# Optimization experiments

Measured on AMD Instinct MI355X. Metric: run time of the kernel, lower is better.

The kernel has to match this reference:

```python
import jax, jax.numpy as jnp
import numpy as np

B, S, HID = 1, 4096, 2048
HQ, HKV, D = 16, 8, 128
G = HQ // HKV
WINDOW = 1024
EPS = 1e-6
ROPE_THETA = 1e6


def setup_inputs() -> dict:
    key = jax.random.key(0)
    ks = jax.random.split(key, 6)
    hidden_states = jax.random.normal(ks[0], (B, S, HID), dtype=jnp.float32)
    Wq = jax.random.normal(ks[1], (HQ * D, HID), dtype=jnp.float32) * 0.02
    Wk = jax.random.normal(ks[2], (HKV * D, HID), dtype=jnp.float32) * 0.02
    Wv = jax.random.normal(ks[3], (HKV * D, HID), dtype=jnp.float32) * 0.02
    Wo = jax.random.normal(ks[4], (HID, HQ * D), dtype=jnp.float32) * 0.02
    q_norm_w = jnp.ones((D,), dtype=jnp.float32)
    k_norm_w = jnp.ones((D,), dtype=jnp.float32)
    # standard RoPE tables
    inv_freq = 1.0 / (ROPE_THETA ** (jnp.arange(0, D, 2, dtype=jnp.float32) / D))
    pos = jnp.arange(S, dtype=jnp.float32)
    freqs = pos[:, None] * inv_freq[None, :]            # [S, D/2]
    emb = jnp.concatenate([freqs, freqs], axis=-1)       # [S, D]
    cos = jnp.cos(emb)[None]                             # [1, S, D]
    sin = jnp.sin(emb)[None]
    return {"hidden_states": hidden_states, "cos": cos, "sin": sin,
            "Wq": Wq, "Wk": Wk, "Wv": Wv, "Wo": Wo,
            "q_norm_w": q_norm_w, "k_norm_w": k_norm_w}


def _rms_norm(x, w):
    var = jnp.mean(jnp.square(x), axis=-1, keepdims=True)
    return w * (x * jax.lax.rsqrt(var + EPS))


def _rotate_half(x):
    x1, x2 = jnp.split(x, 2, axis=-1)
    return jnp.concatenate([-x2, x1], axis=-1)


def reference(hidden_states, cos, sin, Wq, Wk, Wv, Wo, q_norm_w, k_norm_w):
    b, s, _ = hidden_states.shape
    # projections -> [B, H, S, D]
    q = (hidden_states @ Wq.T).reshape(b, s, HQ, D)
    k = (hidden_states @ Wk.T).reshape(b, s, HKV, D)
    v = (hidden_states @ Wv.T).reshape(b, s, HKV, D)
    q = _rms_norm(q, q_norm_w).transpose(0, 2, 1, 3)   # [B,HQ,S,D]
    k = _rms_norm(k, k_norm_w).transpose(0, 2, 1, 3)   # [B,HKV,S,D]
    v = v.transpose(0, 2, 1, 3)
    # RoPE (cos/sin broadcast over head dim)
    c = cos[:, None, :, :]
    sn = sin[:, None, :, :]
    q = q * c + _rotate_half(q) * sn
    k = k * c + _rotate_half(k) * sn
    # GQA: group queries per kv head
    qg = q.reshape(b, HKV, G, s, D)
    scaling = D ** -0.5
    scores = jnp.einsum('bhgqd,bhkd->bhgqk', qg, k) * scaling  # [B,HKV,G,S,S]
    # causal + sliding-window additive mask
    i = jnp.arange(s)[:, None]
    j = jnp.arange(s)[None, :]
    allowed = (j <= i) & (j > i - WINDOW)
    scores = jnp.where(allowed[None, None, None], scores, jnp.float32(-1e9))
    attn = jax.nn.softmax(scores, axis=-1)
    out = jnp.einsum('bhgqk,bhkd->bhgqd', attn, v)     # [B,HKV,G,S,D]
    out = out.reshape(b, HQ, s, D).transpose(0, 2, 1, 3).reshape(b, s, HQ * D)
    return out @ Wo.T
```

## Files before the change

### kernel.cpp

```cpp
#include <hip/hip_runtime.h>

typedef __bf16 bf16;
typedef bf16 bf16x8 __attribute__((ext_vector_type(8)));
typedef bf16 bf16x4 __attribute__((ext_vector_type(4)));
typedef float f32x4 __attribute__((ext_vector_type(4)));

#define MFMA16(a, b, c) __builtin_amdgcn_mfma_f32_16x16x32_bf16((a), (b), (c), 0, 0, 0)

__device__ __forceinline__ void gload_lds16(const bf16* g, bf16* l) {
  __builtin_amdgcn_global_load_lds(
      (const __attribute__((address_space(1))) void*)g,
      (__attribute__((address_space(3))) void*)l, 16, 0, 0);
}

__global__ __launch_bounds__(256) void cvt_f32_bf16(const float* __restrict__ src,
                                                    bf16* __restrict__ dst, int n4) {
  int i = blockIdx.x * blockDim.x + threadIdx.x;
  if (i < n4) {
    float4 v = ((const float4*)src)[i];
    bf16x4 o;
    o[0] = (bf16)v.x; o[1] = (bf16)v.y; o[2] = (bf16)v.z; o[3] = (bf16)v.w;
    ((bf16x4*)dst)[i] = o;
  }
}

template <typename OutT>
__global__ __launch_bounds__(256) void gemm_bt(const bf16* __restrict__ A,
                                               const bf16* __restrict__ B,
                                               OutT* __restrict__ C,
                                               int M, int N, int K) {
  __shared__ __align__(16) bf16 As[128 * 64];
  __shared__ __align__(16) bf16 Bs[128 * 64];
  const int tid = threadIdx.x;
  const int w = tid >> 6, lane = tid & 63;
  const int l15 = lane & 15, quad = lane >> 4;
  const int m0 = blockIdx.y * 128, n0 = blockIdx.x * 128;
  const int wm = (w >> 1) * 64, wn = (w & 1) * 64;

  f32x4 acc[4][4] = {};

  for (int k0 = 0; k0 < K; k0 += 64) {
#pragma unroll
    for (int i = 0; i < 4; i++) {
      int s = w * 256 + i * 64 + lane;
      int row = s >> 3;
      int c8 = (s & 7) ^ (row & 7);
      gload_lds16(A + (size_t)(m0 + row) * K + k0 + c8 * 8, As + (w * 256 + i * 64) * 8);
    }
#pragma unroll
    for (int i = 0; i < 4; i++) {
      int s = w * 256 + i * 64 + lane;
      int row = s >> 3;
      int c8 = (s & 7) ^ (row & 7);
      gload_lds16(B + (size_t)(n0 + row) * K + k0 + c8 * 8, Bs + (w * 256 + i * 64) * 8);
    }
    __syncthreads();

#pragma unroll
    for (int kk = 0; kk < 2; kk++) {
      bf16x8 af[4], bfr[4];
#pragma unroll
      for (int mt = 0; mt < 4; mt++) {
        int row = wm + mt * 16 + l15;
        int slot = row * 8 + ((kk * 4 + quad) ^ (row & 7));
        af[mt] = *(const bf16x8*)(As + slot * 8);
      }
#pragma unroll
      for (int nt = 0; nt < 4; nt++) {
        int row = wn + nt * 16 + l15;
        int slot = row * 8 + ((kk * 4 + quad) ^ (row & 7));
        bfr[nt] = *(const bf16x8*)(Bs + slot * 8);
      }
#pragma unroll
      for (int mt = 0; mt < 4; mt++)
#pragma unroll
        for (int nt = 0; nt < 4; nt++)
          acc[mt][nt] = MFMA16(af[mt], bfr[nt], acc[mt][nt]);
    }
    __syncthreads();
  }

#pragma unroll
  for (int mt = 0; mt < 4; mt++)
#pragma unroll
    for (int nt = 0; nt < 4; nt++) {
      int row = m0 + wm + mt * 16 + quad * 4;
      int col = n0 + wn + nt * 16 + l15;
#pragma unroll
      for (int r = 0; r < 4; r++)
        C[(size_t)(row + r) * N + col] = (OutT)acc[mt][nt][r];
    }
}

__global__ __launch_bounds__(256) void normrope(const bf16* __restrict__ QKVb,
                                                const float* __restrict__ cosb,
                                                const float* __restrict__ sinb,
                                                const float* __restrict__ qw,
                                                const float* __restrict__ kw,
                                                bf16* __restrict__ Qb,
                                                bf16* __restrict__ Kb) {
  const int wid = (blockIdx.x * blockDim.x + threadIdx.x) >> 6;
  const int lane = threadIdx.x & 63;
  const int s = wid / 24;
  const int h = wid % 24;
  const bool isq = (h < 16);
  const int col0 = isq ? h * 128 : 2048 + (h - 16) * 128;
  const float* wt = isq ? qw : kw;

  const bf16* row = QKVb + (size_t)s * 4096 + col0;
  float x1 = (float)row[lane];
  float x2 = (float)row[lane + 64];

  float ss = x1 * x1 + x2 * x2;
#pragma unroll
  for (int m = 32; m >= 1; m >>= 1) ss += __shfl_xor(ss, m, 64);
  float rs = rsqrtf(ss * (1.0f / 128.0f) + 1e-6f);

  float c = cosb[(size_t)s * 128 + lane];
  float sn = sinb[(size_t)s * 128 + lane];
  float xn1 = x1 * rs * wt[lane];
  float xn2 = x2 * rs * wt[lane + 64];
  float o1 = xn1 * c - xn2 * sn;
  float o2 = xn2 * c + xn1 * sn;
  const float scale = isq ? 0.12751652f : 1.0f;
  o1 *= scale; o2 *= scale;

  bf16* dst = isq ? (Qb + ((size_t)h * 4096 + s) * 128)
                  : (Kb + ((size_t)(h - 16) * 4096 + s) * 128);
  dst[lane] = (bf16)o1;
  dst[lane + 64] = (bf16)o2;
}

__global__ __launch_bounds__(256) void vtrans(const bf16* __restrict__ QKVb,
                                              bf16* __restrict__ Vtp) {
  __shared__ __align__(16) bf16 T[64 * 136];
  const int kvh = blockIdx.y;
  const int s0 = blockIdx.x * 64;
  const int tid = threadIdx.x;
  for (int g = tid; g < 1024; g += 256) {
    int s = g >> 4, cg = g & 15;
    *(bf16x8*)(T + s * 136 + cg * 8) =
        *(const bf16x8*)(QKVb + (size_t)(s0 + s) * 4096 + 3072 + kvh * 128 + cg * 8);
  }
  __syncthreads();
  for (int g = tid; g < 1024; g += 256) {
    int d = g >> 3, sg = g & 7;
    bf16x8 v;
#pragma unroll
    for (int j = 0; j < 8; j++) {
      int kp = sg * 8 + j;
      int s = (kp & 3) * 16 + (kp >> 2);
      v[j] = T[s * 136 + d];
    }
    *(bf16x8*)(Vtp + ((size_t)kvh * 128 + d) * 4096 + s0 + sg * 8) = v;
  }
}

__global__ __launch_bounds__(256, 2) void attn_kernel(const bf16* __restrict__ Qb,
                                                      const bf16* __restrict__ Kb,
                                                      const bf16* __restrict__ Vtp,
                                                      bf16* __restrict__ Ob) {
  const int SEQ = 4096, W = 1024;
  const float MP = 17.312340f;
  __shared__ __align__(16) bf16 Ks[64 * 128];
  __shared__ __align__(16) bf16 Vs[128 * 64];
  __shared__ __align__(16) bf16 Ps[4][32 * 64];

  const int id = blockIdx.x;
  const int kvh = id & 7, gq = (id >> 3) & 1, h = kvh * 2 + gq;
  const int qb0 = (id >> 4) * 128;
  const int tid = threadIdx.x, w = tid >> 6, lane = tid & 63;
  const int l15 = lane & 15, quad = lane >> 4;
  const int qw0 = qb0 + w * 32;

  bf16x8 qf[2][4];
#pragma unroll
  for (int m = 0; m < 2; m++) {
    const bf16* qp = Qb + ((size_t)h * SEQ + qw0 + m * 16 + l15) * 128 + quad * 8;
#pragma unroll
    for (int kb = 0; kb < 4; kb++) qf[m][kb] = *(const bf16x8*)(qp + kb * 32);
  }

  f32x4 o[2][8] = {};
  f32x4 lr[2] = {};
  bf16* pw = &Ps[w][0];
  const bf16* kbase = Kb + (size_t)kvh * SEQ * 128;
  const bf16* vbase = Vtp + (size_t)kvh * 128 * SEQ;

  int jmin = qb0 - (W - 1); if (jmin < 0) jmin = 0;
  const int kt0 = jmin >> 6, kt1 = (qb0 + 127) >> 6;

  for (int kt = kt0; kt <= kt1; ++kt) {
    const int k0 = kt * 64;
#pragma unroll
    for (int i = 0; i < 4; i++) {
      int slot = w * 256 + i * 64 + lane;
      int key = slot >> 4, gg = slot & 15;
      int gsw = gg ^ (key & 7);
      gload_lds16(kbase + (size_t)(k0 + key) * 128 + gsw * 8, Ks + (w * 256 + i * 64) * 8);
    }
#pragma unroll
    for (int i = 0; i < 4; i++) {
      int slot = w * 256 + i * 64 + lane;
      int d = slot >> 3, gg = slot & 7;
      int gsw = gg ^ (d & 7);
      gload_lds16(vbase + (size_t)d * SEQ + k0 + gsw * 8, Vs + (w * 256 + i * 64) * 8);
    }
    __syncthreads();

    const bool alive = (k0 <= qw0 + 31) && (k0 + 63 > qw0 - W);
    if (alive) {
      const bool full = (k0 + 63 <= qw0) && (k0 > qw0 + 31 - W);
      f32x4 s[2][4] = {};
#pragma unroll
      for (int c = 0; c < 4; c++) {
        const int key = c * 16 + l15;
        bf16x8 kf[4];
#pragma unroll
        for (int kb = 0; kb < 4; kb++)
          kf[kb] = *(const bf16x8*)(Ks + key * 128 + (((kb * 4 + quad) ^ (key & 7)) << 3));
#pragma unroll
        for (int kb = 0; kb < 4; kb++) {
          s[0][c] = MFMA16(qf[0][kb], kf[kb], s[0][c]);
          s[1][c] = MFMA16(qf[1][kb], kf[kb], s[1][c]);
        }
      }
#pragma unroll
      for (int m = 0; m < 2; m++)
#pragma unroll
        for (int r = 0; r < 4; r++) {
          float p[4];
          if (full) {
#pragma unroll
            for (int c = 0; c < 4; c++) p[c] = __builtin_amdgcn_exp2f(s[m][c][r] - MP);
          } else {
            const int i_ = qw0 + m * 16 + quad * 4 + r;
#pragma unroll
            for (int c = 0; c < 4; c++) {
              int j = k0 + c * 16 + l15;
              p[c] = (j <= i_ && j > i_ - W) ? __builtin_amdgcn_exp2f(s[m][c][r] - MP) : 0.0f;
            }
          }
          lr[m][r] += p[0] + p[1] + p[2] + p[3];
          bf16x4 pk;
          pk[0] = (bf16)p[0]; pk[1] = (bf16)p[1]; pk[2] = (bf16)p[2]; pk[3] = (bf16)p[3];
          const int q = m * 16 + quad * 4 + r;
          *(bf16x4*)(pw + q * 64 + (((l15 >> 1) ^ (q & 7)) << 3) + (l15 & 1) * 4) = pk;
        }
      asm volatile("s_waitcnt lgkmcnt(0)" ::: "memory");
      bf16x8 pf[2][2];
#pragma unroll
      for (int m = 0; m < 2; m++)
#pragma unroll
        for (int kb = 0; kb < 2; kb++)
          pf[m][kb] = *(const bf16x8*)(pw + (m * 16 + l15) * 64 +
                                       (((kb * 4 + quad) ^ (l15 & 7)) << 3));
#pragma unroll
      for (int n = 0; n < 8; n++) {
        const int d = n * 16 + l15;
        bf16x8 vf0 = *(const bf16x8*)(Vs + d * 64 + ((quad ^ (l15 & 7)) << 3));
        bf16x8 vf1 = *(const bf16x8*)(Vs + d * 64 + (((4 + quad) ^ (l15 & 7)) << 3));
        o[0][n] = MFMA16(pf[0][0], vf0, o[0][n]);
        o[0][n] = MFMA16(pf[0][1], vf1, o[0][n]);
        o[1][n] = MFMA16(pf[1][0], vf0, o[1][n]);
        o[1][n] = MFMA16(pf[1][1], vf1, o[1][n]);
      }
    }
    __syncthreads();
  }

  float linv[2][4];
#pragma unroll
  for (int m = 0; m < 2; m++)
#pragma unroll
    for (int r = 0; r < 4; r++) {
      float v = lr[m][r];
      v += __shfl_xor(v, 1, 64);
      v += __shfl_xor(v, 2, 64);
      v += __shfl_xor(v, 4, 64);
      v += __shfl_xor(v, 8, 64);
      linv[m][r] = 1.0f / v;
    }
#pragma unroll
  for (int m = 0; m < 2; m++)
#pragma unroll
    for (int n = 0; n < 8; n++)
#pragma unroll
      for (int r = 0; r < 4; r++) {
        int i_ = qw0 + m * 16 + quad * 4 + r;
        Ob[(size_t)i_ * 2048 + h * 128 + n * 16 + l15] = (bf16)(o[m][n][r] * linv[m][r]);
      }
}

extern "C" void kernel_launch(void* const* d_in, const int* in_sizes, int n_in,
                              void* d_out, int out_size, void* d_ws, size_t ws_size,
                              hipStream_t stream) {
  const float* hid  = (const float*)d_in[0];
  const float* cosb = (const float*)d_in[1];
  const float* sinb = (const float*)d_in[2];
  const float* Wq   = (const float*)d_in[3];
  const float* Wk   = (const float*)d_in[4];
  const float* Wv   = (const float*)d_in[5];
  const float* Wo   = (const float*)d_in[6];
  const float* qw   = (const float*)d_in[7];
  const float* kw   = (const float*)d_in[8];

  if (ws_size < (size_t)(112u) * 1024u * 1024u) return;

  char* ws = (char*)d_ws;
  bf16* Xbf  = (bf16*)(ws);
  bf16* Vtp  = (bf16*)(ws);
  bf16* Wcat = (bf16*)(ws + (16u << 20));
  bf16* Wob  = (bf16*)(ws + (32u << 20));
  bf16* QKVb = (bf16*)(ws + (40u << 20));
  bf16* Qb   = (bf16*)(ws + (72u << 20));
  bf16* Kb   = (bf16*)(ws + (88u << 20));
  bf16* Ob   = (bf16*)(ws + (96u << 20));

  cvt_f32_bf16<<<8192, 256, 0, stream>>>(hid, Xbf, 2097152);
  cvt_f32_bf16<<<4096, 256, 0, stream>>>(Wq, Wcat, 1048576);
  cvt_f32_bf16<<<2048, 256, 0, stream>>>(Wk, Wcat + 4194304, 524288);
  cvt_f32_bf16<<<2048, 256, 0, stream>>>(Wv, Wcat + 6291456, 524288);
  cvt_f32_bf16<<<4096, 256, 0, stream>>>(Wo, Wob, 1048576);

  gemm_bt<bf16><<<dim3(32, 32), 256, 0, stream>>>(Xbf, Wcat, QKVb, 4096, 4096, 2048);
  vtrans<<<dim3(64, 8), 256, 0, stream>>>(QKVb, Vtp);
  normrope<<<24576, 256, 0, stream>>>(QKVb, cosb, sinb, qw, kw, Qb, Kb);
  attn_kernel<<<512, 256, 0, stream>>>(Qb, Kb, Vtp, Ob);
  gemm_bt<float><<<dim3(16, 32), 256, 0, stream>>>(Ob, Wob, (float*)d_out, 4096, 2048, 2048);
}
```

Before: 339.3 us.

## Use 256x256-tile pipelined GEMM for the QKV projection

Adds a new 512-thread GEMM kernel with 256x256 output tiles, a 4-slot LDS ring buffer loaded via global_load_lds, split A/B prefetch interleaved with MFMA phases, s_setprio around the MFMA bursts, and a workgroup-index remap for L2 locality. It replaces the 128x128 gemm_bt for the QKV projection to raise operand reuse per LDS byte and hide global-load latency. The cost is larger LDS use (128KB per block) and heavier register use, which limits occupancy and may leave CUs idle since only 256 blocks are launched. A local variable in the attention kernel is also renamed so it does not shadow the new name.

After: 328.9 us. 1.03x faster.

```diff
diff --git a/kernel.cpp b/kernel.cpp
--- a/kernel.cpp
+++ b/kernel.cpp
@@ -89,6 +89,121 @@
 #pragma unroll
       for (int r = 0; r < 4; r++)
         C[(size_t)(row + r) * N + col] = (OutT)acc[mt][nt][r];
+    }
+}
+
+__global__ __launch_bounds__(512, 2) void gemm256_bt(const bf16* __restrict__ A,
+                                                     const bf16* __restrict__ B,
+                                                     bf16* __restrict__ C,
+                                                     int M, int N, int K) {
+  __shared__ __align__(16) bf16 SA[4][8192];
+  __shared__ __align__(16) bf16 SB[4][8192];
+  const int NT = K >> 5;
+  const int tid = threadIdx.x;
+  const int w = tid >> 6, lane = tid & 63;
+  const int l15 = lane & 15, quad = lane >> 4;
+  const int wr = w >> 2, wc = w & 3;
+
+  const int nbx = N >> 8;
+  const int nwg = (M >> 8) * nbx;
+  const int wg = ((int)blockIdx.x & 7) * (nwg >> 3) + ((int)blockIdx.x >> 3);
+  const int bm0 = (wg / nbx) << 8;
+  const int bn0 = (wg % nbx) << 8;
+
+  const int q = tid >> 3, p = tid & 7;
+  const int u = p ^ (q & 7);
+  const int srow = 2 * q + (u >> 2);
+  const int sg = u & 3;
+  const bf16* sA0 = A + (size_t)(bm0 + srow) * K + sg * 8;
+  const bf16* sA1 = sA0 + (size_t)128 * K;
+  const bf16* sB0 = B + (size_t)(bn0 + srow) * K + sg * 8;
+  const bf16* sB1 = sB0 + (size_t)128 * K;
+  const int dst = w * 512;
+
+  const int pA = (((l15 & 1) << 2) + quad) ^ (l15 >> 1);
+  const int aoff = wr * 4096 + (l15 >> 1) * 64 + pA * 8;
+  const int boff = (wc >> 1) * 4096 + (wc & 1) * 2048 + (l15 >> 1) * 64 + pA * 8;
+
+  f32x4 acc[8][4] = {};
+
+#pragma unroll
+  for (int tt = 0; tt < 2; ++tt) {
+    gload_lds16(sA0 + tt * 32, &SA[tt][0] + dst);
+    gload_lds16(sA1 + tt * 32, &SA[tt][4096] + dst);
+    gload_lds16(sB0 + tt * 32, &SB[tt][0] + dst);
+    gload_lds16(sB1 + tt * 32, &SB[tt][4096] + dst);
+  }
+  asm volatile("s_waitcnt vmcnt(4)" ::: "memory");
+  __builtin_amdgcn_sched_barrier(0);
+  __builtin_amdgcn_s_barrier();
+  __builtin_amdgcn_sched_barrier(0);
+
+  for (int t = 0; t < NT; ++t) {
+    const bf16* sa = &SA[t & 3][0];
+    const bf16* sb = &SB[t & 3][0];
+    const int ts = t + 2;
+    const int sl = ts & 3;
+
+    bf16x8 bfr[4], af[4];
+#pragma unroll
+    for (int nt = 0; nt < 4; ++nt) bfr[nt] = *(const bf16x8*)(sb + boff + nt * 512);
+#pragma unroll
+    for (int mt = 0; mt < 4; ++mt) af[mt] = *(const bf16x8*)(sa + aoff + mt * 512);
+    if (ts < NT) {
+      gload_lds16(sA0 + ts * 32, &SA[sl][0] + dst);
+      gload_lds16(sA1 + ts * 32, &SA[sl][4096] + dst);
+    }
+    __builtin_amdgcn_sched_barrier(0);
+    __builtin_amdgcn_s_barrier();
+    asm volatile("s_waitcnt lgkmcnt(0)" ::: "memory");
+    __builtin_amdgcn_sched_barrier(0);
+    __builtin_amdgcn_s_setprio(1);
+#pragma unroll
+    for (int mt = 0; mt < 4; ++mt)
+#pragma unroll
+      for (int nt = 0; nt < 4; ++nt)
+        acc[mt][nt] = MFMA16(af[mt], bfr[nt], acc[mt][nt]);
+    __builtin_amdgcn_s_setprio(0);
+    __builtin_amdgcn_sched_barrier(0);
+    __builtin_amdgcn_s_barrier();
+    __builtin_amdgcn_sched_barrier(0);
+
+#pragma unroll
+    for (int mt = 0; mt < 4; ++mt) af[mt] = *(const bf16x8*)(sa + aoff + (mt + 4) * 512);
+    if (ts < NT) {
+      gload_lds16(sB0 + ts * 32, &SB[sl][0] + dst);
+      gload_lds16(sB1 + ts * 32, &SB[sl][4096] + dst);
+    }
+    __builtin_amdgcn_sched_barrier(0);
+    __builtin_amdgcn_s_barrier();
+    asm volatile("s_waitcnt lgkmcnt(0)" ::: "memory");
+    __builtin_amdgcn_sched_barrier(0);
+    __builtin_amdgcn_s_setprio(1);
+#pragma unroll
+    for (int mt = 0; mt < 4; ++mt)
+#pragma unroll
+      for (int nt = 0; nt < 4; ++nt)
+        acc[mt + 4][nt] = MFMA16(af[mt], bfr[nt], acc[mt + 4][nt]);
+    __builtin_amdgcn_s_setprio(0);
+    if (ts < NT) {
+      asm volatile("s_waitcnt vmcnt(4)" ::: "memory");
+    } else {
+      asm volatile("s_waitcnt vmcnt(0)" ::: "memory");
+    }
+    __builtin_amdgcn_sched_barrier(0);
+    __builtin_amdgcn_s_barrier();
+    __builtin_amdgcn_sched_barrier(0);
+  }
+
+#pragma unroll
+  for (int mt = 0; mt < 8; ++mt)
+#pragma unroll
+    for (int nt = 0; nt < 4; ++nt) {
+      int row = bm0 + wr * 128 + mt * 16 + quad * 4;
+      int col = bn0 + wc * 64 + nt * 16 + l15;
+#pragma unroll
+      for (int r = 0; r < 4; ++r)
+        C[(size_t)(row + r) * N + col] = (bf16)acc[mt][nt][r];
     }
 }
 
@@ -244,8 +359,8 @@
           lr[m][r] += p[0] + p[1] + p[2] + p[3];
           bf16x4 pk;
           pk[0] = (bf16)p[0]; pk[1] = (bf16)p[1]; pk[2] = (bf16)p[2]; pk[3] = (bf16)p[3];
-          const int q = m * 16 + quad * 4 + r;
-          *(bf16x4*)(pw + q * 64 + (((l15 >> 1) ^ (q & 7)) << 3) + (l15 & 1) * 4) = pk;
+          const int qrow = m * 16 + quad * 4 + r;
+          *(bf16x4*)(pw + qrow * 64 + (((l15 >> 1) ^ (qrow & 7)) << 3) + (l15 & 1) * 4) = pk;
         }
       asm volatile("s_waitcnt lgkmcnt(0)" ::: "memory");
       bf16x8 pf[2][2];
@@ -323,7 +438,7 @@
   cvt_f32_bf16<<<2048, 256, 0, stream>>>(Wv, Wcat + 6291456, 524288);
   cvt_f32_bf16<<<4096, 256, 0, stream>>>(Wo, Wob, 1048576);
 
-  gemm_bt<bf16><<<dim3(32, 32), 256, 0, stream>>>(Xbf, Wcat, QKVb, 4096, 4096, 2048);
+  gemm256_bt<<<256, 512, 0, stream>>>(Xbf, Wcat, QKVb, 4096, 4096, 2048);
   vtrans<<<dim3(64, 8), 256, 0, stream>>>(QKVb, Vtp);
   normrope<<<24576, 256, 0, stream>>>(QKVb, cosb, sinb, qw, kw, Qb, Kb);
   attn_kernel<<<512, 256, 0, stream>>>(Qb, Kb, Vtp, Ob);
```

## Replace GEMM with double-buffered, software-pipelined 512-thread larger-tile kernel

Applied to the files above, without the earlier changes.

Replaces the simple single-buffered 128x128 GEMM with a templated kernel that double-buffers the LDS tiles and uses 8 waves per block. It overlaps global-to-LDS loads of the next K tile with MFMA work on the current one, using explicit waitcnt, sched_barrier and setprio to interleave the phases. Tiles grow to 256x256 for the QKV projection and 128x256 for the output projection, and workgroups are remapped so they cover the output in an XCD-aware order. This adds register pressure and relies on hand-tuned wait counts, which are fragile if the unrolled load counts change.

Measured after the change: 325.4 us. -4.1%, faster.

```diff
diff --git a/kernel.cpp b/kernel.cpp
--- a/kernel.cpp
+++ b/kernel.cpp
@@ -11,6 +11,19 @@
   __builtin_amdgcn_global_load_lds(
       (const __attribute__((address_space(1))) void*)g,
       (__attribute__((address_space(3))) void*)l, 16, 0, 0);
+}
+
+template <int N>
+__device__ __forceinline__ void lgkm_fence() {
+  if constexpr (N == 0) asm volatile("s_waitcnt lgkmcnt(0)" ::: "memory");
+  else if constexpr (N == 4) asm volatile("s_waitcnt lgkmcnt(4)" ::: "memory");
+  else if constexpr (N == 8) asm volatile("s_waitcnt lgkmcnt(8)" ::: "memory");
+  else if constexpr (N == 12) asm volatile("s_waitcnt lgkmcnt(12)" ::: "memory");
+  __builtin_amdgcn_sched_barrier(0);
+}
+__device__ __forceinline__ void bar_fence() {
+  __builtin_amdgcn_sched_barrier(0);
+  __builtin_amdgcn_s_barrier();
 }
 
 __global__ __launch_bounds__(256) void cvt_f32_bf16(const float* __restrict__ src,
@@ -24,70 +37,138 @@
   }
 }
 
-template <typename OutT>
-__global__ __launch_bounds__(256) void gemm_bt(const bf16* __restrict__ A,
-                                               const bf16* __restrict__ B,
-                                               OutT* __restrict__ C,
-                                               int M, int N, int K) {
-  __shared__ __align__(16) bf16 As[128 * 64];
-  __shared__ __align__(16) bf16 Bs[128 * 64];
+template <int BM, int BN, int MT, int NTT, typename OutT>
+__global__ __launch_bounds__(512, 2) void gemm_pipe(const bf16* __restrict__ A,
+                                                    const bf16* __restrict__ B,
+                                                    OutT* __restrict__ C,
+                                                    int M, int N, int K) {
+  constexpr int MH = MT / 2, NH = NTT / 2;
+  constexpr int ASLOT = BM * 64;
+  constexpr int BSLOT = BN * 64;
+  constexpr int NLA = BM / 64, NLB = BN / 64;
+  __shared__ __align__(16) bf16 SA[2 * ASLOT];
+  __shared__ __align__(16) bf16 SB[2 * BSLOT];
+
+  const int NTILES = K >> 6;
   const int tid = threadIdx.x;
   const int w = tid >> 6, lane = tid & 63;
   const int l15 = lane & 15, quad = lane >> 4;
-  const int m0 = blockIdx.y * 128, n0 = blockIdx.x * 128;
-  const int wm = (w >> 1) * 64, wn = (w & 1) * 64;
-
-  f32x4 acc[4][4] = {};
-
-  for (int k0 = 0; k0 < K; k0 += 64) {
-#pragma unroll
-    for (int i = 0; i < 4; i++) {
-      int s = w * 256 + i * 64 + lane;
-      int row = s >> 3;
-      int c8 = (s & 7) ^ (row & 7);
-      gload_lds16(A + (size_t)(m0 + row) * K + k0 + c8 * 8, As + (w * 256 + i * 64) * 8);
-    }
-#pragma unroll
-    for (int i = 0; i < 4; i++) {
-      int s = w * 256 + i * 64 + lane;
-      int row = s >> 3;
-      int c8 = (s & 7) ^ (row & 7);
-      gload_lds16(B + (size_t)(n0 + row) * K + k0 + c8 * 8, Bs + (w * 256 + i * 64) * 8);
-    }
-    __syncthreads();
-
-#pragma unroll
-    for (int kk = 0; kk < 2; kk++) {
-      bf16x8 af[4], bfr[4];
-#pragma unroll
-      for (int mt = 0; mt < 4; mt++) {
-        int row = wm + mt * 16 + l15;
-        int slot = row * 8 + ((kk * 4 + quad) ^ (row & 7));
-        af[mt] = *(const bf16x8*)(As + slot * 8);
-      }
-#pragma unroll
-      for (int nt = 0; nt < 4; nt++) {
-        int row = wn + nt * 16 + l15;
-        int slot = row * 8 + ((kk * 4 + quad) ^ (row & 7));
-        bfr[nt] = *(const bf16x8*)(Bs + slot * 8);
-      }
-#pragma unroll
-      for (int mt = 0; mt < 4; mt++)
-#pragma unroll
-        for (int nt = 0; nt < 4; nt++)
-          acc[mt][nt] = MFMA16(af[mt], bfr[nt], acc[mt][nt]);
-    }
-    __syncthreads();
-  }
-
-#pragma unroll
-  for (int mt = 0; mt < 4; mt++)
-#pragma unroll
-    for (int nt = 0; nt < 4; nt++) {
-      int row = m0 + wm + mt * 16 + quad * 4;
-      int col = n0 + wn + nt * 16 + l15;
-#pragma unroll
-      for (int r = 0; r < 4; r++)
+  const int wr = w >> 2, wc = w & 3;
+
+  const int nbx = N / BN;
+  const int nwg = (M / BM) * nbx;
+  const int wg = ((int)blockIdx.x & 7) * (nwg >> 3) + ((int)blockIdx.x >> 3);
+  const int bm0 = (wg / nbx) * BM;
+  const int bn0 = (wg % nbx) * BN;
+
+  const int r0 = tid >> 3;
+  const int sg = (tid & 7) ^ ((tid >> 3) & 7);
+  unsigned aoffg[NLA], boffg[NLB];
+#pragma unroll
+  for (int i = 0; i < NLA; ++i)
+    aoffg[i] = (unsigned)((bm0 + r0 + i * 64) * K + sg * 8);
+#pragma unroll
+  for (int i = 0; i < NLB; ++i)
+    boffg[i] = (unsigned)((bn0 + r0 + i * 64) * K + sg * 8);
+
+  const int xl = l15 & 7;
+  const int p0 = quad ^ xl;
+  const int baseA0 = (wr * (MT * 16) + l15) * 128 + p0 * 16;
+  const int baseA1 = (wr * (MT * 16) + l15) * 128 + ((p0 ^ 4) * 16);
+  const int baseB0 = (wc * (NTT * 16) + l15) * 128 + p0 * 16;
+  const int baseB1 = (wc * (NTT * 16) + l15) * 128 + ((p0 ^ 4) * 16);
+  const char* saB = (const char*)&SA[0];
+  const char* sbB = (const char*)&SB[0];
+
+  f32x4 acc[MT][NTT] = {};
+  bf16x8 As[2][MH][2];
+  bf16x8 Bs[2][NH][2];
+
+#define LDA_(SL, H, DST)                                                        \
+  _Pragma("unroll") for (int mt = 0; mt < MH; ++mt) {                           \
+    (DST)[mt][0] = *(const bf16x8*)(saB + (SL) * (ASLOT * 2) + baseA0 +         \
+                                    ((H) * MH + mt) * 2048);                    \
+    (DST)[mt][1] = *(const bf16x8*)(saB + (SL) * (ASLOT * 2) + baseA1 +         \
+                                    ((H) * MH + mt) * 2048);                    \
+  }
+#define LDB_(SL, G, DST)                                                        \
+  _Pragma("unroll") for (int nt = 0; nt < NH; ++nt) {                           \
+    (DST)[nt][0] = *(const bf16x8*)(sbB + (SL) * (BSLOT * 2) + baseB0 +         \
+                                    ((G) * NH + nt) * 2048);                    \
+    (DST)[nt][1] = *(const bf16x8*)(sbB + (SL) * (BSLOT * 2) + baseB1 +         \
+                                    ((G) * NH + nt) * 2048);                    \
+  }
+#define QMFMA_(AS, BS, MHI, NHI)                                                \
+  __builtin_amdgcn_s_setprio(1);                                                \
+  _Pragma("unroll") for (int mt = 0; mt < MH; ++mt)                             \
+      _Pragma("unroll") for (int nt = 0; nt < NH; ++nt) {                       \
+    acc[(MHI) * MH + mt][(NHI) * NH + nt] = MFMA16(                             \
+        (AS)[mt][0], (BS)[nt][0], acc[(MHI) * MH + mt][(NHI) * NH + nt]);       \
+    acc[(MHI) * MH + mt][(NHI) * NH + nt] = MFMA16(                             \
+        (AS)[mt][1], (BS)[nt][1], acc[(MHI) * MH + mt][(NHI) * NH + nt]);       \
+  }                                                                             \
+  __builtin_amdgcn_s_setprio(0);
+#define STAGE_(SO, TS)                                                          \
+  _Pragma("unroll") for (int i = 0; i < NLA; ++i)                               \
+      gload_lds16(A + aoffg[i] + (TS) * 64, SA + (SO) * ASLOT + tid * 8 + i * 4096); \
+  _Pragma("unroll") for (int i = 0; i < NLB; ++i)                               \
+      gload_lds16(B + boffg[i] + (TS) * 64, SB + (SO) * BSLOT + tid * 8 + i * 4096);
+
+#define GTILE_BODY(PAR, TS)                                                     \
+  {                                                                             \
+    constexpr int sl_ = (PAR), so_ = (PAR) ^ 1;                                 \
+    constexpr int e0_ = (PAR), e1_ = (PAR) ^ 1;                                 \
+                                                                        \
+    LDB_(sl_, 1, Bs[e1_]);                                                      \
+    bar_fence();                                                                \
+    lgkm_fence<NTT>();                                                          \
+    if ((TS) < NTILES) { STAGE_(so_, (TS)); }                                   \
+    QMFMA_(As[0], Bs[e0_], 0, 0);                                               \
+                                                                        \
+    LDA_(sl_, 1, As[1]);                                                        \
+    bar_fence();                                                                \
+    lgkm_fence<MT>();                                                           \
+    QMFMA_(As[0], Bs[e1_], 0, 1);                                               \
+                                                                        \
+    LDB_(sl_, 0, Bs[e0_]);                                                      \
+    asm volatile("s_waitcnt vmcnt(0)" ::: "memory");                            \
+    bar_fence();                                                                \
+    lgkm_fence<NTT>();                                                          \
+    QMFMA_(As[1], Bs[e1_], 1, 1);                                               \
+                                                                        \
+    LDA_(so_, 0, As[0]);                                                        \
+    LDB_(so_, 0, Bs[e1_]);                                                      \
+    bar_fence();                                                                \
+    lgkm_fence<MT + NTT>();                                                     \
+    QMFMA_(As[1], Bs[e0_], 1, 0);                                               \
+  }
+
+  { STAGE_(0, 0); }
+  asm volatile("s_waitcnt vmcnt(0)" ::: "memory");
+  bar_fence();
+  __builtin_amdgcn_sched_barrier(0);
+  LDA_(0, 0, As[0]);
+  LDB_(0, 0, Bs[0]);
+
+  for (int t = 0; t < NTILES; t += 2) {
+    GTILE_BODY(0, t + 1);
+    GTILE_BODY(1, t + 2);
+  }
+
+#undef LDA_
+#undef LDB_
+#undef QMFMA_
+#undef STAGE_
+#undef GTILE_BODY
+
+#pragma unroll
+  for (int mt = 0; mt < MT; ++mt)
+#pragma unroll
+    for (int nt = 0; nt < NTT; ++nt) {
+      int row = bm0 + wr * (MT * 16) + mt * 16 + quad * 4;
+      int col = bn0 + wc * (NTT * 16) + nt * 16 + l15;
+#pragma unroll
+      for (int r = 0; r < 4; ++r)
         C[(size_t)(row + r) * N + col] = (OutT)acc[mt][nt][r];
     }
 }
@@ -244,8 +325,8 @@
           lr[m][r] += p[0] + p[1] + p[2] + p[3];
           bf16x4 pk;
           pk[0] = (bf16)p[0]; pk[1] = (bf16)p[1]; pk[2] = (bf16)p[2]; pk[3] = (bf16)p[3];
-          const int q = m * 16 + quad * 4 + r;
-          *(bf16x4*)(pw + q * 64 + (((l15 >> 1) ^ (q & 7)) << 3) + (l15 & 1) * 4) = pk;
+          const int qrow = m * 16 + quad * 4 + r;
+          *(bf16x4*)(pw + qrow * 64 + (((l15 >> 1) ^ (qrow & 7)) << 3) + (l15 & 1) * 4) = pk;
         }
       asm volatile("s_waitcnt lgkmcnt(0)" ::: "memory");
       bf16x8 pf[2][2];
@@ -323,9 +404,9 @@
   cvt_f32_bf16<<<2048, 256, 0, stream>>>(Wv, Wcat + 6291456, 524288);
   cvt_f32_bf16<<<4096, 256, 0, stream>>>(Wo, Wob, 1048576);
 
-  gemm_bt<bf16><<<dim3(32, 32), 256, 0, stream>>>(Xbf, Wcat, QKVb, 4096, 4096, 2048);
+  gemm_pipe<256, 256, 8, 4, bf16><<<256, 512, 0, stream>>>(Xbf, Wcat, QKVb, 4096, 4096, 2048);
   vtrans<<<dim3(64, 8), 256, 0, stream>>>(QKVb, Vtp);
   normrope<<<24576, 256, 0, stream>>>(QKVb, cosb, sinb, qw, kw, Qb, Kb);
   attn_kernel<<<512, 256, 0, stream>>>(Qb, Kb, Vtp, Ob);
-  gemm_bt<float><<<dim3(16, 32), 256, 0, stream>>>(Ob, Wob, (float*)d_out, 4096, 2048, 2048);
-}
+  gemm_pipe<128, 256, 4, 4, float><<<256, 512, 0, stream>>>(Ob, Wob, (float*)d_out, 4096, 2048, 2048);
+}
```

## Replace GEMMs with 8-wave double-buffered pipelined kernel with larger tiles

Applied to the files above, without the earlier changes.

Replaces the simple single-buffered 128x128 GEMM with an 8-wave, 256-wide N tile kernel. It double-buffers LDS with global_load_lds prefetch two k-tiles ahead and interleaves quadrant MFMA phases with barriers and setprio. It also remaps workgroup IDs so neighbouring blocks share tiles in cache. The aim is to hide global-load latency and raise MFMA utilisation in the QKV and output projections, at the cost of more LDS, more registers and a more fragile schedule.

After: 333.6 us. Within noise of the previous version (-1.7%).

```diff
diff --git a/kernel.cpp b/kernel.cpp
--- a/kernel.cpp
+++ b/kernel.cpp
@@ -12,6 +12,20 @@
       (const __attribute__((address_space(1))) void*)g,
       (__attribute__((address_space(3))) void*)l, 16, 0, 0);
 }
+
+template <int N>
+__device__ __forceinline__ void lgkm_fence() {
+  if constexpr (N == 0) asm volatile("s_waitcnt lgkmcnt(0)" ::: "memory");
+  else asm volatile("s_waitcnt lgkmcnt(8)" ::: "memory");
+  __builtin_amdgcn_sched_barrier(0);
+}
+
+#define BARX()                                  \
+  do {                                          \
+    __builtin_amdgcn_sched_barrier(0);          \
+    __builtin_amdgcn_s_barrier();               \
+    __builtin_amdgcn_sched_barrier(0);          \
+  } while (0)
 
 __global__ __launch_bounds__(256) void cvt_f32_bf16(const float* __restrict__ src,
                                                     bf16* __restrict__ dst, int n4) {
@@ -24,72 +38,172 @@
   }
 }
 
-template <typename OutT>
-__global__ __launch_bounds__(256) void gemm_bt(const bf16* __restrict__ A,
-                                               const bf16* __restrict__ B,
-                                               OutT* __restrict__ C,
-                                               int M, int N, int K) {
-  __shared__ __align__(16) bf16 As[128 * 64];
-  __shared__ __align__(16) bf16 Bs[128 * 64];
+template <int BM, typename OutT>
+__global__ __launch_bounds__(512, 2) void gemm8p(const bf16* __restrict__ A,
+                                                 const bf16* __restrict__ B,
+                                                 OutT* __restrict__ C,
+                                                 int M, int N, int K) {
+  static_assert(BM == 256 || BM == 128, "");
+  constexpr int MT = BM / 32;
+  constexpr int AQ = MT / 2;
+  constexpr int AHALF = (BM / 2) * 64;
+  constexpr int BHALF = 128 * 64;
+  constexpr int NLA = BM / 128;
+  constexpr int NLB = 2;
+  constexpr int VMC = 2 * NLA + NLB;
+
+  __shared__ __align__(16) bf16 SA[2 * 2 * AHALF];
+  __shared__ __align__(16) bf16 SB[2 * 2 * BHALF];
+
+  const int NT = K >> 6;
   const int tid = threadIdx.x;
   const int w = tid >> 6, lane = tid & 63;
   const int l15 = lane & 15, quad = lane >> 4;
-  const int m0 = blockIdx.y * 128, n0 = blockIdx.x * 128;
-  const int wm = (w >> 1) * 64, wn = (w & 1) * 64;
-
-  f32x4 acc[4][4] = {};
-
-  for (int k0 = 0; k0 < K; k0 += 64) {
-#pragma unroll
-    for (int i = 0; i < 4; i++) {
-      int s = w * 256 + i * 64 + lane;
-      int row = s >> 3;
-      int c8 = (s & 7) ^ (row & 7);
-      gload_lds16(A + (size_t)(m0 + row) * K + k0 + c8 * 8, As + (w * 256 + i * 64) * 8);
-    }
-#pragma unroll
-    for (int i = 0; i < 4; i++) {
-      int s = w * 256 + i * 64 + lane;
-      int row = s >> 3;
-      int c8 = (s & 7) ^ (row & 7);
-      gload_lds16(B + (size_t)(n0 + row) * K + k0 + c8 * 8, Bs + (w * 256 + i * 64) * 8);
-    }
-    __syncthreads();
-
-#pragma unroll
-    for (int kk = 0; kk < 2; kk++) {
-      bf16x8 af[4], bfr[4];
-#pragma unroll
-      for (int mt = 0; mt < 4; mt++) {
-        int row = wm + mt * 16 + l15;
-        int slot = row * 8 + ((kk * 4 + quad) ^ (row & 7));
-        af[mt] = *(const bf16x8*)(As + slot * 8);
-      }
-#pragma unroll
-      for (int nt = 0; nt < 4; nt++) {
-        int row = wn + nt * 16 + l15;
-        int slot = row * 8 + ((kk * 4 + quad) ^ (row & 7));
-        bfr[nt] = *(const bf16x8*)(Bs + slot * 8);
-      }
-#pragma unroll
-      for (int mt = 0; mt < 4; mt++)
-#pragma unroll
-        for (int nt = 0; nt < 4; nt++)
-          acc[mt][nt] = MFMA16(af[mt], bfr[nt], acc[mt][nt]);
-    }
-    __syncthreads();
-  }
-
-#pragma unroll
-  for (int mt = 0; mt < 4; mt++)
-#pragma unroll
-    for (int nt = 0; nt < 4; nt++) {
-      int row = m0 + wm + mt * 16 + quad * 4;
-      int col = n0 + wn + nt * 16 + l15;
-#pragma unroll
-      for (int r = 0; r < 4; r++)
-        C[(size_t)(row + r) * N + col] = (OutT)acc[mt][nt][r];
-    }
+  const int wr = w >> 2, wc = w & 3;
+
+  const int nbx = N >> 8;
+  const int nwg = (M / BM) * nbx;
+  const int wg = ((int)blockIdx.x & 7) * (nwg >> 3) + ((int)blockIdx.x >> 3);
+  const int bm0 = (wg / nbx) * BM;
+  const int bn0 = (wg % nbx) << 8;
+
+  const bf16* apt[NLA];
+  const bf16* bpt[NLB];
+#pragma unroll
+  for (int i = 0; i < NLA; ++i) {
+    int s = i * 512 + tid, r = s >> 3, g = (s & 7) ^ (r & 7);
+    apt[i] = A + (size_t)(bm0 + r) * K + g * 8;
+  }
+#pragma unroll
+  for (int i = 0; i < NLB; ++i) {
+    int s = i * 512 + tid, r = s >> 3, g = (s & 7) ^ (r & 7);
+    bpt[i] = B + (size_t)(bn0 + r) * K + g * 8;
+  }
+  const size_t hsA = (size_t)(BM / 2) * K;
+  const size_t hsB = (size_t)128 * K;
+
+  int aoff[AQ][2], boff[2][2];
+#pragma unroll
+  for (int m = 0; m < AQ; ++m) {
+    int lr = wr * (BM / 4) + m * 16 + l15;
+#pragma unroll
+    for (int ks = 0; ks < 2; ++ks)
+      aoff[m][ks] = lr * 64 + (((ks * 4 + quad) ^ (lr & 7)) << 3);
+  }
+#pragma unroll
+  for (int nq = 0; nq < 2; ++nq) {
+    int lc = wc * 32 + nq * 16 + l15;
+#pragma unroll
+    for (int ks = 0; ks < 2; ++ks)
+      boff[nq][ks] = lc * 64 + (((ks * 4 + quad) ^ (lc & 7)) << 3);
+  }
+
+  f32x4 acc[MT][4] = {};
+  bf16x8 af[AQ][2], bfA[2][2], bfB[2][2];
+
+#define STAGE_A_(H, SO, KT)                                                     \
+  _Pragma("unroll") for (int i_ = 0; i_ < NLA; ++i_)                            \
+      gload_lds16(apt[i_] + (H) * hsA + (KT) * 64,                              \
+                  SA + ((SO) * 2 + (H)) * AHALF + i_ * 4096 + tid * 8)
+#define STAGE_B_(H, SO, KT)                                                     \
+  _Pragma("unroll") for (int i_ = 0; i_ < NLB; ++i_)                            \
+      gload_lds16(bpt[i_] + (H) * hsB + (KT) * 64,                              \
+                  SB + ((SO) * 2 + (H)) * BHALF + i_ * 4096 + tid * 8)
+#define LDAQ_(QM, SL)                                                           \
+  _Pragma("unroll") for (int m_ = 0; m_ < AQ; ++m_)                             \
+      _Pragma("unroll") for (int k_ = 0; k_ < 2; ++k_)                          \
+          af[m_][k_] = *(const bf16x8*)(SA + ((SL) * 2 + (QM)) * AHALF + aoff[m_][k_])
+#define LDBQ_(QN, SL, DST)                                                      \
+  _Pragma("unroll") for (int n_ = 0; n_ < 2; ++n_)                              \
+      _Pragma("unroll") for (int k_ = 0; k_ < 2; ++k_)                          \
+          DST[n_][k_] = *(const bf16x8*)(SB + ((SL) * 2 + (QN)) * BHALF + boff[n_][k_])
+#define MFQ_(QM, QN, BF)                                                        \
+  do {                                                                          \
+    __builtin_amdgcn_s_setprio(1);                                              \
+    _Pragma("unroll") for (int k_ = 0; k_ < 2; ++k_)                            \
+        _Pragma("unroll") for (int m_ = 0; m_ < AQ; ++m_)                       \
+            _Pragma("unroll") for (int n_ = 0; n_ < 2; ++n_)                    \
+                acc[(QM) * AQ + m_][(QN) * 2 + n_] =                            \
+                    MFMA16(af[m_][k_], BF[n_][k_],                              \
+                           acc[(QM) * AQ + m_][(QN) * 2 + n_]);                 \
+    __builtin_amdgcn_s_setprio(0);                                              \
+  } while (0)
+
+#define TILE_(T, STG1, STG2, VMM)                                               \
+  do {                                                                          \
+    const int sl_ = (T) & 1, so_ = sl_ ^ 1;                                     \
+                                                      \
+    LDAQ_(0, sl_);                                                              \
+    LDBQ_(0, sl_, bfA);                                                         \
+    if (STG1) { STAGE_B_(0, so_, (T) + 1); }                                    \
+    if constexpr (AQ == 4) { asm volatile("s_waitcnt lgkmcnt(8)" ::: "memory"); } \
+    BARX();                                                                     \
+    lgkm_fence<0>();                                                            \
+    MFQ_(0, 0, bfA);                                                            \
+    BARX();                                                                     \
+                                                               \
+    LDBQ_(1, sl_, bfB);                                                         \
+    if (STG2) { STAGE_A_(0, sl_, (T) + 2); }                                    \
+    BARX();                                                                     \
+    lgkm_fence<0>();                                                            \
+    MFQ_(0, 1, bfB);                                                            \
+    BARX();                                                                     \
+                                                               \
+    LDAQ_(1, sl_);                                                              \
+    if (STG2) { STAGE_B_(1, sl_, (T) + 2); }                                    \
+    BARX();                                                                     \
+    lgkm_fence<0>();                                                            \
+    MFQ_(1, 1, bfB);                                                            \
+    BARX();                                                                     \
+                                                   \
+    LDBQ_(0, sl_, bfA);                                                         \
+    if (STG2) { STAGE_A_(1, sl_, (T) + 2); }                                    \
+    BARX();                                                                     \
+    lgkm_fence<0>();                                                            \
+    MFQ_(1, 0, bfA);                                                            \
+    if ((VMM) == 1) { asm volatile("s_waitcnt vmcnt(%0)" :: "i"(VMC) : "memory"); } \
+    else if ((VMM) == 2) { asm volatile("s_waitcnt vmcnt(0)" ::: "memory"); }   \
+    BARX();                                                                     \
+  } while (0)
+
+  STAGE_A_(0, 0, 0);
+  STAGE_B_(0, 0, 0);
+  STAGE_A_(1, 0, 0);
+  STAGE_B_(1, 0, 0);
+  STAGE_A_(0, 1, 1);
+  STAGE_B_(1, 1, 1);
+  STAGE_A_(1, 1, 1);
+  asm volatile("s_waitcnt vmcnt(%0)" :: "i"(VMC) : "memory");
+  BARX();
+
+  int t = 0;
+  for (; t < NT - 2; ++t) TILE_(t, 1, 1, 1);
+  TILE_(t, 1, 0, 2);
+  ++t;
+  TILE_(t, 0, 0, 0);
+
+#undef STAGE_A_
+#undef STAGE_B_
+#undef LDAQ_
+#undef LDBQ_
+#undef MFQ_
+#undef TILE_
+
+#pragma unroll
+  for (int qm = 0; qm < 2; ++qm)
+#pragma unroll
+    for (int m = 0; m < AQ; ++m)
+#pragma unroll
+      for (int qn = 0; qn < 2; ++qn)
+#pragma unroll
+        for (int n = 0; n < 2; ++n) {
+          int row = bm0 + qm * (BM / 2) + wr * (BM / 4) + m * 16 + quad * 4;
+          int col = bn0 + qn * 128 + wc * 32 + n * 16 + l15;
+          f32x4 v = acc[qm * AQ + m][qn * 2 + n];
+#pragma unroll
+          for (int r = 0; r < 4; ++r)
+            C[(size_t)(row + r) * N + col] = (OutT)v[r];
+        }
 }
 
 __global__ __launch_bounds__(256) void normrope(const bf16* __restrict__ QKVb,
@@ -244,8 +358,8 @@
           lr[m][r] += p[0] + p[1] + p[2] + p[3];
           bf16x4 pk;
           pk[0] = (bf16)p[0]; pk[1] = (bf16)p[1]; pk[2] = (bf16)p[2]; pk[3] = (bf16)p[3];
-          const int q = m * 16 + quad * 4 + r;
-          *(bf16x4*)(pw + q * 64 + (((l15 >> 1) ^ (q & 7)) << 3) + (l15 & 1) * 4) = pk;
+          const int qrow = m * 16 + quad * 4 + r;
+          *(bf16x4*)(pw + qrow * 64 + (((l15 >> 1) ^ (qrow & 7)) << 3) + (l15 & 1) * 4) = pk;
         }
       asm volatile("s_waitcnt lgkmcnt(0)" ::: "memory");
       bf16x8 pf[2][2];
@@ -323,9 +437,9 @@
   cvt_f32_bf16<<<2048, 256, 0, stream>>>(Wv, Wcat + 6291456, 524288);
   cvt_f32_bf16<<<4096, 256, 0, stream>>>(Wo, Wob, 1048576);
 
-  gemm_bt<bf16><<<dim3(32, 32), 256, 0, stream>>>(Xbf, Wcat, QKVb, 4096, 4096, 2048);
+  gemm8p<256, bf16><<<256, 512, 0, stream>>>(Xbf, Wcat, QKVb, 4096, 4096, 2048);
   vtrans<<<dim3(64, 8), 256, 0, stream>>>(QKVb, Vtp);
   normrope<<<24576, 256, 0, stream>>>(QKVb, cosb, sinb, qw, kw, Qb, Kb);
   attn_kernel<<<512, 256, 0, stream>>>(Qb, Kb, Vtp, Ob);
-  gemm_bt<float><<<dim3(16, 32), 256, 0, stream>>>(Ob, Wob, (float*)d_out, 4096, 2048, 2048);
-}
+  gemm8p<128, float><<<256, 512, 0, stream>>>(Ob, Wob, (float*)d_out, 4096, 2048, 2048);
+}
```
